# Optimization experiments

Hardware: AMD Instinct MI355X
Metric: run time of the kernel (lower is better)

Reference implementation:

```python
import jax, jax.numpy as jnp
import numpy as np

DIM = 1024
HEADS = 16
DIM_HEAD = 64
DIM_INNER = HEADS * DIM_HEAD  # 1024


def setup_inputs() -> dict:
    key = jax.random.key(0)
    k1, k2, k3 = jax.random.split(key, 3)
    x = jax.random.normal(k1, (2, 2048, DIM), dtype=jnp.float32)
    gamma = jnp.zeros((DIM,), dtype=jnp.float32)  # init as in module
    # store weights as [in, out] so y = x @ W (equivalent to torch Linear with W.T)
    w_qkv = jax.random.normal(k2, (DIM, DIM_INNER * 3), dtype=jnp.float32) * (DIM ** -0.5)
    w_out = jax.random.normal(k3, (DIM_INNER, DIM), dtype=jnp.float32) * (DIM_INNER ** -0.5)
    return {"x": x, "gamma": gamma, "w_qkv": w_qkv, "w_out": w_out}


def rms_norm(x, gamma):
    # F.normalize(x, dim=-1) * sqrt(dim) * (gamma + 1)
    eps = 1e-12
    norm = jnp.maximum(jnp.linalg.norm(x, axis=-1, keepdims=True), eps)
    return x / norm * (x.shape[-1] ** 0.5) * (gamma + 1.0)


def reference(x, gamma, w_qkv, w_out):
    b, n, _ = x.shape
    scale = DIM_HEAD ** -0.5
    xn = rms_norm(x, gamma)
    qkv = xn @ w_qkv  # [b, n, 3*h*d]
    qkv = qkv.reshape(b, n, 3, HEADS, DIM_HEAD)
    qkv = jnp.transpose(qkv, (2, 0, 3, 1, 4))  # [3, b, h, n, d]
    q, k, v = qkv[0], qkv[1], qkv[2]
    q = q * scale
    sim = jnp.einsum('bhid,bhjd->bhij', q, k)
    attn = jax.nn.softmax(sim, axis=-1)
    out = jnp.einsum('bhij,bhjd->bhid', attn, v)  # [b, h, n, d]
    out = jnp.transpose(out, (0, 2, 1, 3)).reshape(b, n, DIM_INNER)
    return out @ w_out
```

## Files before the change

kernel.cpp:

```cpp
#include <hip/hip_runtime.h>
#include <hip/hip_bf16.h>

typedef unsigned short ushort_t;
typedef __attribute__((ext_vector_type(8))) short short8;
typedef __attribute__((ext_vector_type(4))) short short4v;
typedef __attribute__((ext_vector_type(4))) float floatx4;
typedef __attribute__((ext_vector_type(4))) int int4v;
typedef __attribute__((ext_vector_type(4))) unsigned short us4;

#define MFMA(a, b, c) __builtin_amdgcn_mfma_f32_16x16x32_bf16(a, b, c, 0, 0, 0)
#define MFMA16(a, b, c) __builtin_amdgcn_mfma_f32_16x16x16bf16_1k(a, b, c, 0, 0, 0)

__device__ __forceinline__ float b2f(ushort_t u) {
    union { float f; unsigned i; } c; c.i = ((unsigned)u) << 16; return c.f;
}
__device__ __forceinline__ ushort_t f2b(float f) {
    union { float f; unsigned i; } c; c.f = f;
    unsigned r = c.i + 0x7FFFu + ((c.i >> 16) & 1u);
    return (ushort_t)(r >> 16);
}
__device__ __forceinline__ ushort_t f2b_fast(float f) {
    union { float f; unsigned i; } c; c.f = f;
    return (ushort_t)((c.i + 0x8000u) >> 16);
}

__global__ __launch_bounds__(256) void rmsnorm_k(const float* __restrict__ x,
                                                 const float* __restrict__ gamma,
                                                 ushort_t* __restrict__ xn) {
    int row = blockIdx.x;
    const float* xr = x + (size_t)row * 1024;
    ushort_t* orow = xn + (size_t)row * 1024;
    int t = threadIdx.x;

    floatx4 u = *(const floatx4*)&xr[t * 4];
    float ss = u[0] * u[0] + u[1] * u[1] + u[2] * u[2] + u[3] * u[3];
    #pragma unroll
    for (int off = 32; off; off >>= 1) ss += __shfl_xor(ss, off);
    __shared__ float red[4];
    if ((t & 63) == 0) red[t >> 6] = ss;
    __syncthreads();
    float tot = red[0] + red[1] + red[2] + red[3];
    float inv = rsqrtf(fmaxf(tot, 1e-24f)) * 32.0f;

    floatx4 g = *(const floatx4*)&gamma[t * 4];
    us4 o;
    o.x = f2b(u[0] * inv * (1.0f + g[0]));
    o.y = f2b(u[1] * inv * (1.0f + g[1]));
    o.z = f2b(u[2] * inv * (1.0f + g[2]));
    o.w = f2b(u[3] * inv * (1.0f + g[3]));
    *(us4*)&orow[t * 4] = o;
}

__global__ __launch_bounds__(256) void transpose_cvt_k(const float* __restrict__ in,
                                                       ushort_t* __restrict__ out,
                                                       int K, int N) {
    __shared__ ushort_t Ts[64 * 72];
    int t = threadIdx.x;
    int n0 = blockIdx.x * 64, k0 = blockIdx.y * 64;
    #pragma unroll
    for (int i = 0; i < 4; i++) {
        int idx = t + i * 256;
        int r = idx >> 4, g = idx & 15;
        floatx4 v = *(const floatx4*)&in[(size_t)(k0 + r) * N + n0 + g * 4];
        us4 o; o.x = f2b(v[0]); o.y = f2b(v[1]); o.z = f2b(v[2]); o.w = f2b(v[3]);
        *(us4*)&Ts[r * 72 + g * 4] = o;
    }
    __syncthreads();
    #pragma unroll
    for (int i = 0; i < 2; i++) {
        int idx = t + i * 256;
        int r = idx >> 3, g = idx & 7;
        ushort_t tmp[8];
        #pragma unroll
        for (int j = 0; j < 8; j++) tmp[j] = Ts[(g * 8 + j) * 72 + r];
        *(int4v*)&out[(size_t)(n0 + r) * K + k0 + g * 8] = *(const int4v*)tmp;
    }
}

#define LDK 72
template <bool F32OUT>
__global__ __launch_bounds__(256) void gemm_tn(const ushort_t* __restrict__ A,
                                               const ushort_t* __restrict__ Bt,
                                               void* __restrict__ Cv,
                                               int M, int N, int K) {
    __shared__ ushort_t As[128 * LDK];
    __shared__ ushort_t Bs[128 * LDK];
    int t = threadIdx.x;
    int m0 = blockIdx.y * 128, n0 = blockIdx.x * 128;
    int lane = t & 63, wave = t >> 6, quad = lane >> 4, l16 = lane & 15;
    int wm = (wave & 1) * 64, wn = (wave >> 1) * 64;
    floatx4 acc[4][4] = {};

    for (int k1 = 0; k1 < K; k1 += 64) {
        __syncthreads();
        #pragma unroll
        for (int i = 0; i < 4; i++) {
            int idx = t + i * 256;
            int r = idx >> 3, g = idx & 7;
            *(int4v*)&As[r * LDK + g * 8] =
                *(const int4v*)&A[(size_t)(m0 + r) * K + k1 + g * 8];
            *(int4v*)&Bs[r * LDK + g * 8] =
                *(const int4v*)&Bt[(size_t)(n0 + r) * K + k1 + g * 8];
        }
        __syncthreads();
        #pragma unroll
        for (int ks = 0; ks < 2; ks++) {
            short8 af[4], bf[4];
            #pragma unroll
            for (int i = 0; i < 4; i++) {
                af[i] = *(const short8*)&As[(wm + i * 16 + l16) * LDK + ks * 32 + quad * 8];
                bf[i] = *(const short8*)&Bs[(wn + i * 16 + l16) * LDK + ks * 32 + quad * 8];
            }
            #pragma unroll
            for (int mt = 0; mt < 4; mt++)
                #pragma unroll
                for (int nt = 0; nt < 4; nt++)
                    acc[mt][nt] = MFMA(af[mt], bf[nt], acc[mt][nt]);
        }
    }
    #pragma unroll
    for (int mt = 0; mt < 4; mt++)
        #pragma unroll
        for (int r = 0; r < 4; r++) {
            int row = m0 + wm + mt * 16 + quad * 4 + r;
            #pragma unroll
            for (int nt = 0; nt < 4; nt++) {
                int col = n0 + wn + nt * 16 + l16;
                if constexpr (F32OUT)
                    ((float*)Cv)[(size_t)row * N + col] = acc[mt][nt][r];
                else
                    ((ushort_t*)Cv)[(size_t)row * N + col] = f2b(acc[mt][nt][r]);
            }
        }
}

#define LDA 72
__global__ __launch_bounds__(256, 2) void attn_k(const ushort_t* __restrict__ qk,
                                                 const ushort_t* __restrict__ vT,
                                                 ushort_t* __restrict__ o) {
    __shared__ ushort_t Ks[64 * LDA];
    __shared__ ushort_t Vt[64 * LDA];
    int t = threadIdx.x;
    int lane = t & 63, wave = t >> 6, quad = lane >> 4, l16 = lane & 15;
    int bid = blockIdx.x;
    int bh = bid & 31, qb = bid >> 5;
    int b = bh >> 4, h = bh & 15;
    int q0 = qb * 128 + wave * 32;
    const size_t RS = 2048;
    const ushort_t* Qb = qk + (size_t)b * 2048 * RS + h * 64;
    const ushort_t* Kb = Qb + 1024;
    const ushort_t* Vb = vT + (size_t)(h * 64) * 4096 + b * 2048;
    const float SC = 0.18033688011112042f;

    int srow = t >> 2, sseg = t & 3;

    short8 qf[2][2];
    #pragma unroll
    for (int qt = 0; qt < 2; qt++)
        #pragma unroll
        for (int ks = 0; ks < 2; ks++) {
            union { short8 s; ushort_t u[8]; } a;
            a.s = *(const short8*)&Qb[(size_t)(q0 + qt * 16 + l16) * RS + ks * 32 + quad * 8];
            #pragma unroll
            for (int j = 0; j < 8; j++) a.u[j] = f2b(b2f(a.u[j]) * SC);
            qf[qt][ks] = a.s;
        }

    short4v ones4;
    #pragma unroll
    for (int j = 0; j < 4; j++) ones4[j] = (short)0x3F80;

    floatx4 oacc[2][4] = {};
    floatx4 sum_acc[2] = {};

    for (int kt = 0; kt < 2048; kt += 64) {
        __syncthreads();
        *(int4v*)&Ks[srow * LDA + sseg * 8] =
            *(const int4v*)&Kb[(size_t)(kt + srow) * RS + sseg * 8];
        *(int4v*)&Ks[srow * LDA + 32 + sseg * 8] =
            *(const int4v*)&Kb[(size_t)(kt + srow) * RS + 32 + sseg * 8];
        *(int4v*)&Vt[srow * LDA + sseg * 8] =
            *(const int4v*)&Vb[(size_t)srow * 4096 + kt + sseg * 8];
        *(int4v*)&Vt[srow * LDA + 32 + sseg * 8] =
            *(const int4v*)&Vb[(size_t)srow * 4096 + kt + 32 + sseg * 8];
        __syncthreads();

        floatx4 s[2][4];
        #pragma unroll
        for (int mt = 0; mt < 4; mt++) {
            short8 kf0 = *(const short8*)&Ks[(mt * 16 + l16) * LDA + quad * 8];
            short8 kf1 = *(const short8*)&Ks[(mt * 16 + l16) * LDA + 32 + quad * 8];
            #pragma unroll
            for (int qt = 0; qt < 2; qt++) {
                floatx4 z = {};
                z = MFMA(kf0, qf[qt][0], z);
                s[qt][mt] = MFMA(kf1, qf[qt][1], z);
            }
        }

        short4v pa[2][4];
        #pragma unroll
        for (int qt = 0; qt < 2; qt++)
            #pragma unroll
            for (int mt = 0; mt < 4; mt++)
                #pragma unroll
                for (int r = 0; r < 4; r++)
                    pa[qt][mt][r] = (short)f2b_fast(exp2f(fminf(s[qt][mt][r], 50.0f)));

        #pragma unroll
        for (int mt = 0; mt < 4; mt++) {
            short4v vb[4];
            #pragma unroll
            for (int dt = 0; dt < 4; dt++)
                vb[dt] = *(const short4v*)&Vt[(dt * 16 + l16) * LDA + mt * 16 + quad * 4];
            #pragma unroll
            for (int qt = 0; qt < 2; qt++) {
                sum_acc[qt] = MFMA16(pa[qt][mt], ones4, sum_acc[qt]);
                #pragma unroll
                for (int dt = 0; dt < 4; dt++)
                    oacc[qt][dt] = MFMA16(pa[qt][mt], vb[dt], oacc[qt][dt]);
            }
        }
    }

    ushort_t* ob = o + (size_t)b * 2048 * 1024 + h * 64;
    #pragma unroll
    for (int qt = 0; qt < 2; qt++)
        #pragma unroll
        for (int r = 0; r < 4; r++) {
            float inv = 1.0f / sum_acc[qt][r];
            int row = q0 + qt * 16 + quad * 4 + r;
            #pragma unroll
            for (int dt = 0; dt < 4; dt++)
                ob[(size_t)row * 1024 + dt * 16 + l16] = f2b(oacc[qt][dt][r] * inv);
        }
}

extern "C" void kernel_launch(void* const* d_in, const int* in_sizes, int n_in,
                              void* d_out, int out_size, void* d_ws, size_t ws_size,
                              hipStream_t stream) {
    const float* x     = (const float*)d_in[0];
    const float* gamma = (const float*)d_in[1];
    const float* w_qkv = (const float*)d_in[2];
    const float* w_out = (const float*)d_in[3];
    float* out = (float*)d_out;

    ushort_t* ws   = (ushort_t*)d_ws;
    ushort_t* xn   = ws;
    ushort_t* qkb  = xn + (size_t)4096 * 1024;
    ushort_t* vTb  = qkb + (size_t)4096 * 2048;
    ushort_t* wtq  = vTb + (size_t)1024 * 4096;
    ushort_t* wto  = wtq + (size_t)3072 * 1024;
    ushort_t* attn = xn;

    rmsnorm_k<<<4096, 256, 0, stream>>>(x, gamma, xn);
    transpose_cvt_k<<<dim3(48, 16), 256, 0, stream>>>(w_qkv, wtq, 1024, 3072);
    transpose_cvt_k<<<dim3(16, 16), 256, 0, stream>>>(w_out, wto, 1024, 1024);
    gemm_tn<false><<<dim3(16, 32), 256, 0, stream>>>(xn, wtq, qkb, 4096, 2048, 1024);
    gemm_tn<false><<<dim3(32, 8), 256, 0, stream>>>(wtq + (size_t)2048 * 1024, xn, vTb,
                                                    1024, 4096, 1024);
    attn_k<<<512, 256, 0, stream>>>(qkb, vTb, attn);
    gemm_tn<true><<<dim3(8, 32), 256, 0, stream>>>(attn, wto, out, 4096, 1024, 1024);
}
```

Before: 222.4 us.

## Load GEMM tiles directly global-to-LDS with XOR swizzle; pack bf16 exp conversion

The GEMM now fills shared memory with global_load_lds (direct global-to-LDS DMA) instead of loading into registers and storing. It drops the padded LDS stride in favour of an XOR-swizzled chunk layout to avoid bank conflicts, and moves the barrier to the end of each k-iteration. In attention, the exp results are converted to bf16 in pairs with the packed round-to-nearest intrinsic, and the clamp at 50 is removed. Removing the clamp could risk overflow if scores are large, and the swizzle indexing must match exactly between writes and reads.

```diff
diff --git a/kernel.cpp b/kernel.cpp
--- a/kernel.cpp
+++ b/kernel.cpp
@@ -1,5 +1,6 @@
 #include <hip/hip_runtime.h>
 #include <hip/hip_bf16.h>
+#include <string.h>
 
 typedef unsigned short ushort_t;
 typedef __attribute__((ext_vector_type(8))) short short8;
@@ -19,9 +20,17 @@
     unsigned r = c.i + 0x7FFFu + ((c.i >> 16) & 1u);
     return (ushort_t)(r >> 16);
 }
-__device__ __forceinline__ ushort_t f2b_fast(float f) {
-    union { float f; unsigned i; } c; c.f = f;
-    return (ushort_t)((c.i + 0x8000u) >> 16);
+__device__ __forceinline__ unsigned pk_bf16(float a, float b) {
+    float2 f; f.x = a; f.y = b;
+    __hip_bfloat162 h = __float22bfloat162_rn(f);
+    unsigned u;
+    memcpy(&u, &h, 4);
+    return u;
+}
+__device__ __forceinline__ void gl_lds16(const ushort_t* g, ushort_t* l) {
+    __builtin_amdgcn_global_load_lds(
+        (const __attribute__((address_space(1))) void*)g,
+        (__attribute__((address_space(3))) void*)l, 16, 0, 0);
 }
 
 __global__ __launch_bounds__(256) void rmsnorm_k(const float* __restrict__ x,
@@ -77,39 +86,42 @@
     }
 }
 
-#define LDK 72
 template <bool F32OUT>
 __global__ __launch_bounds__(256) void gemm_tn(const ushort_t* __restrict__ A,
                                                const ushort_t* __restrict__ Bt,
                                                void* __restrict__ Cv,
                                                int M, int N, int K) {
-    __shared__ ushort_t As[128 * LDK];
-    __shared__ ushort_t Bs[128 * LDK];
+    __shared__ ushort_t As[128 * 64];
+    __shared__ ushort_t Bs[128 * 64];
     int t = threadIdx.x;
     int m0 = blockIdx.y * 128, n0 = blockIdx.x * 128;
     int lane = t & 63, wave = t >> 6, quad = lane >> 4, l16 = lane & 15;
     int wm = (wave & 1) * 64, wn = (wave >> 1) * 64;
     floatx4 acc[4][4] = {};
 
+    int srow = lane >> 3;
+    int schunk = (lane & 7) ^ srow;
+    const ushort_t* Ag = A + (size_t)(m0 + wave * 8 + srow) * K + schunk * 8;
+    const ushort_t* Bg = Bt + (size_t)(n0 + wave * 8 + srow) * K + schunk * 8;
+    int lbase = (wave * 8) * 64;
+
+    int xq = l16 & 7;
+
     for (int k1 = 0; k1 < K; k1 += 64) {
-        __syncthreads();
         #pragma unroll
         for (int i = 0; i < 4; i++) {
-            int idx = t + i * 256;
-            int r = idx >> 3, g = idx & 7;
-            *(int4v*)&As[r * LDK + g * 8] =
-                *(const int4v*)&A[(size_t)(m0 + r) * K + k1 + g * 8];
-            *(int4v*)&Bs[r * LDK + g * 8] =
-                *(const int4v*)&Bt[(size_t)(n0 + r) * K + k1 + g * 8];
+            gl_lds16(Ag + (size_t)(i * 32) * K + k1, &As[lbase + i * 32 * 64]);
+            gl_lds16(Bg + (size_t)(i * 32) * K + k1, &Bs[lbase + i * 32 * 64]);
         }
         __syncthreads();
         #pragma unroll
         for (int ks = 0; ks < 2; ks++) {
+            int ca = ((ks * 4 + quad) ^ xq) * 8;
             short8 af[4], bf[4];
             #pragma unroll
             for (int i = 0; i < 4; i++) {
-                af[i] = *(const short8*)&As[(wm + i * 16 + l16) * LDK + ks * 32 + quad * 8];
-                bf[i] = *(const short8*)&Bs[(wn + i * 16 + l16) * LDK + ks * 32 + quad * 8];
+                af[i] = *(const short8*)&As[(wm + i * 16 + l16) * 64 + ca];
+                bf[i] = *(const short8*)&Bs[(wn + i * 16 + l16) * 64 + ca];
             }
             #pragma unroll
             for (int mt = 0; mt < 4; mt++)
@@ -117,6 +129,7 @@
                 for (int nt = 0; nt < 4; nt++)
                     acc[mt][nt] = MFMA(af[mt], bf[nt], acc[mt][nt]);
         }
+        __syncthreads();
     }
     #pragma unroll
     for (int mt = 0; mt < 4; mt++)
@@ -202,10 +215,12 @@
         #pragma unroll
         for (int qt = 0; qt < 2; qt++)
             #pragma unroll
-            for (int mt = 0; mt < 4; mt++)
-                #pragma unroll
-                for (int r = 0; r < 4; r++)
-                    pa[qt][mt][r] = (short)f2b_fast(exp2f(fminf(s[qt][mt][r], 50.0f)));
+            for (int mt = 0; mt < 4; mt++) {
+                union { short4v v; unsigned u[2]; } pk;
+                pk.u[0] = pk_bf16(exp2f(s[qt][mt][0]), exp2f(s[qt][mt][1]));
+                pk.u[1] = pk_bf16(exp2f(s[qt][mt][2]), exp2f(s[qt][mt][3]));
+                pa[qt][mt] = pk.v;
+            }
 
         #pragma unroll
         for (int mt = 0; mt < 4; mt++) {
```

Result: no change. 223.5 us (+0.5%).
